# Performance work log

Measured on AMD Instinct MI355X. Metric: run time of the kernel, lower is better.

## Reference

```python
import jax, jax.numpy as jnp
import numpy as np

B, T, I, H, O = 4096, 512, 1, 64, 1


def setup_inputs() -> dict:
    key = jax.random.key(0)
    ks = jax.random.split(key, 7)
    s = 1.0 / np.sqrt(H)  # PyTorch default init scale
    return {
        "x": jax.random.normal(ks[0], (B, T, I), dtype=jnp.float32),
        "w_ih": jax.random.uniform(ks[1], (4 * H, I), jnp.float32, -s, s),
        "w_hh": jax.random.uniform(ks[2], (4 * H, H), jnp.float32, -s, s),
        "b_ih": jax.random.uniform(ks[3], (4 * H,), jnp.float32, -s, s),
        "b_hh": jax.random.uniform(ks[4], (4 * H,), jnp.float32, -s, s),
        "w_out": jax.random.uniform(ks[5], (O, H), jnp.float32, -s, s),
        "b_out": jax.random.uniform(ks[6], (O,), jnp.float32, -s, s),
    }


def reference(x, w_ih, w_hh, b_ih, b_hh, w_out, b_out):
    # x: [B, T, I]; PyTorch gate order in 4H dim is (i, f, g, o)
    b = b_ih + b_hh  # [4H]
    # precompute input projections for all timesteps: [T, B, 4H]
    xg = jnp.einsum("bti,gi->tbg", x, w_ih) + b

    def step(carry, xg_t):
        h, c = carry  # [B, H] each
        gates = xg_t + h @ w_hh.T  # [B, 4H]
        i, f, g, o = jnp.split(gates, 4, axis=-1)
        i = jax.nn.sigmoid(i)
        f = jax.nn.sigmoid(f)
        g = jnp.tanh(g)
        o = jax.nn.sigmoid(o)
        c = f * c + i * g
        h = o * jnp.tanh(c)
        return (h, c), None

    nb = x.shape[0]
    h0 = jnp.zeros((nb, w_hh.shape[1]), x.dtype)
    (h_T, _), _ = jax.lax.scan(step, (h0, h0), xg)
    # linear on last hidden state only (lstm_out[:, -1, :])
    return h_T @ w_out.T + b_out
```

## Files before the change

kernel.cpp:

```cpp
#include <hip/hip_runtime.h>


#define TT   512
#define MB   8
#define HP   72
#define BUFE (16 * HP)
#define SXP  10

#define L2E  1.4426950408889634f
#define L2E2 2.8853900817779268f

typedef _Float16 f16x8 __attribute__((ext_vector_type(8)));
typedef float    f32x4 __attribute__((ext_vector_type(4)));
typedef float    f32x2 __attribute__((ext_vector_type(2)));

#define MFMA16(a, b, c) __builtin_amdgcn_mfma_f32_16x16x32_f16((a), (b), (c), 0, 0, 0)

__device__ __forceinline__ float rcp_(float x)  { return __builtin_amdgcn_rcpf(x); }
__device__ __forceinline__ float exp2_(float x) { return __builtin_amdgcn_exp2f(x); }

__device__ __forceinline__ f16x8 cvt8s(const float4& u0, const float4& u1, float s) {
    f16x8 r;
    r[0] = (_Float16)(u0.x * s); r[1] = (_Float16)(u0.y * s);
    r[2] = (_Float16)(u0.z * s); r[3] = (_Float16)(u0.w * s);
    r[4] = (_Float16)(u1.x * s); r[5] = (_Float16)(u1.y * s);
    r[6] = (_Float16)(u1.z * s); r[7] = (_Float16)(u1.w * s);
    return r;
}

__global__ __launch_bounds__(256, 2) void lstm_mfma(
    const float* __restrict__ x,
    const float* __restrict__ w_ih,
    const float* __restrict__ w_hh,
    const float* __restrict__ b_ih,
    const float* __restrict__ b_hh,
    const float* __restrict__ w_out,
    const float* __restrict__ b_out,
    float* __restrict__ out)
{
    __shared__ __align__(16) float    sh_x[TT * SXP];
    __shared__ __align__(16) _Float16 hbuf[2 * BUFE];

    const int tid = threadIdx.x;
    const int w   = tid >> 6;
    const int L   = tid & 63;
    const int l16 = L & 15;
    const int h0  = L >> 4;
    const int b0  = blockIdx.x * MB;
    const int j   = 16 * w + l16;

    {
        const int q = tid >> 5;
        const int l = tid & 31;
        const float* xr = x + (size_t)(b0 + q) * TT;
        #pragma unroll
        for (int i = 0; i < TT / 32; ++i)
            sh_x[(l + 32 * i) * SXP + q] = xr[l + 32 * i];
    }
    for (int i = tid; i < 2 * BUFE; i += 256) hbuf[i] = (_Float16)0.0f;

    const float sc[4] = {-L2E, -L2E, L2E2, -L2E};
    f16x8 Bf[4][2];
    float wihv[4], biasv[4];
    #pragma unroll
    for (int s = 0; s < 4; ++s) {
        const int n = 64 * s + j;
        #pragma unroll
        for (int kt = 0; kt < 2; ++kt) {
            const float* p = w_hh + n * 64 + kt * 32 + h0 * 8;
            float4 u0 = *(const float4*)p;
            float4 u1 = *(const float4*)(p + 4);
            Bf[s][kt] = cvt8s(u0, u1, sc[s]);
        }
        wihv[s]  = w_ih[n] * sc[s];
        biasv[s] = (b_ih[n] + b_hh[n]) * sc[s];
    }

    const int aoff = l16 * HP + h0 * 8;
    const int xoff = 2 * h0;
    const int wr   = 4 * h0 * HP + j;

    f32x2 ccv = {0.0f, 0.0f};

    f32x4 ci[4];
    {
        const float2 x0 = *(const float2*)(sh_x + xoff);
        #pragma unroll
        for (int s = 0; s < 4; ++s) {
            ci[s][0] = fmaf(x0.x, wihv[s], biasv[s]);
            ci[s][1] = 0.0f;
            ci[s][2] = fmaf(x0.y, wihv[s], biasv[s]);
            ci[s][3] = 0.0f;
        }
    }

    __syncthreads();

    if (((blockIdx.x >> 8) ^ blockIdx.x) & 1) {
        __builtin_amdgcn_s_sleep(10);
    }

    auto step = [&](const _Float16* rb, _Float16* wb, int t) {
        f16x8 a0 = *(const f16x8*)(rb + aoff);
        f16x8 a1 = *(const f16x8*)(rb + aoff + 32);

        f32x4 acc[4];
        #pragma unroll
        for (int s = 0; s < 4; ++s)
            acc[s] = MFMA16(a1, Bf[s][1], MFMA16(a0, Bf[s][0], ci[s]));

        if (t + 1 < TT) {
            const float2 xn = *(const float2*)(sh_x + (t + 1) * SXP + xoff);
            const f32x2 xnv = {xn.x, xn.y};
            #pragma unroll
            for (int s = 0; s < 4; ++s) {
                f32x2 c2 = xnv * wihv[s] + biasv[s];
                ci[s][0] = c2[0];
                ci[s][2] = c2[1];
            }
        }

        __builtin_amdgcn_s_setprio(1);

        f32x2 Ei = {exp2_(acc[0][0]), exp2_(acc[0][2])};
        f32x2 Ef = {exp2_(acc[1][0]), exp2_(acc[1][2])};
        f32x2 Eg = {exp2_(acc[2][0]), exp2_(acc[2][2])};
        f32x2 Eo = {exp2_(acc[3][0]), exp2_(acc[3][2])};
        f32x2 Di = Ei + 1.0f, Df = Ef + 1.0f, Dg = Eg + 1.0f, Do = Eo + 1.0f;

        f32x2 FG = Df * Dg, IG = Di * Dg, IF = Di * Df;
        f32x2 P  = Di * FG;
        float u  = rcp_(P[0] * P[1]);
        f32x2 inv = {u * P[1], u * P[0]};

        f32x2 si = FG * inv, sf = IG * inv;
        f32x2 tg = 1.0f - 2.0f * (IF * inv);
        ccv = sf * ccv + si * tg;

        f32x2 ca = ccv * L2E2;
        f32x2 Ec = {exp2_(fminf(ca[0], 30.0f)), exp2_(fminf(ca[1], 30.0f))};
        f32x2 Dc = Ec + 1.0f;
        f32x2 Q  = Do * Dc;
        float v  = rcp_(Q[0] * Q[1]);
        f32x2 iq = {v * Q[1], v * Q[0]};
        f32x2 hv = (iq * Dc) * (1.0f - 2.0f * (iq * Do));

        wb[wr]          = (_Float16)hv[0];
        wb[wr + 2 * HP] = (_Float16)hv[1];

        __builtin_amdgcn_s_setprio(0);
        __syncthreads();
    };

    for (int t = 0; t < TT; t += 2) {
        step(hbuf,        hbuf + BUFE, t);
        step(hbuf + BUFE, hbuf,        t + 1);
    }

    const float wo = w_out[L];
    #pragma unroll
    for (int p = 0; p < 2; ++p) {
        const int q = 2 * w + p;
        float v = (float)hbuf[(2 * q) * HP + L] * wo;
        #pragma unroll
        for (int off = 32; off; off >>= 1) v += __shfl_down(v, off);
        if (L == 0) out[b0 + q] = v + b_out[0];
    }
}

extern "C" void kernel_launch(void* const* d_in, const int* in_sizes, int n_in,
                              void* d_out, int out_size, void* d_ws, size_t ws_size,
                              hipStream_t stream) {
    const float* x     = (const float*)d_in[0];
    const float* w_ih  = (const float*)d_in[1];
    const float* w_hh  = (const float*)d_in[2];
    const float* b_ih  = (const float*)d_in[3];
    const float* b_hh  = (const float*)d_in[4];
    const float* w_out = (const float*)d_in[5];
    const float* b_out = (const float*)d_in[6];
    float* out = (float*)d_out;

    lstm_mfma<<<4096 / MB, 256, 0, stream>>>(x, w_ih, w_hh, b_ih, b_hh,
                                             w_out, b_out, out);
}
```

Baseline: 265.9 us.

## Fill all 16 MFMA rows with batch elements, halving block count

```diff
diff --git a/kernel.cpp b/kernel.cpp
--- a/kernel.cpp
+++ b/kernel.cpp
@@ -2,10 +2,10 @@
 
 
 #define TT   512
-#define MB   8
+#define MB   16
 #define HP   72
 #define BUFE (16 * HP)
-#define SXP  10
+#define SXP  20
 
 #define L2E  1.4426950408889634f
 #define L2E2 2.8853900817779268f
@@ -28,7 +28,7 @@
     return r;
 }
 
-__global__ __launch_bounds__(256, 2) void lstm_mfma(
+__global__ __launch_bounds__(256, 1) void lstm_mfma(
     const float* __restrict__ x,
     const float* __restrict__ w_ih,
     const float* __restrict__ w_hh,
@@ -49,8 +49,9 @@
     const int b0  = blockIdx.x * MB;
     const int j   = 16 * w + l16;
 
-    {
-        const int q = tid >> 5;
+    #pragma unroll
+    for (int rep = 0; rep < 2; ++rep) {
+        const int q = (tid >> 5) + 8 * rep;
         const int l = tid & 31;
         const float* xr = x + (size_t)(b0 + q) * TT;
         #pragma unroll
@@ -77,28 +78,25 @@
     }
 
     const int aoff = l16 * HP + h0 * 8;
-    const int xoff = 2 * h0;
+    const int xb   = 4 * h0;
     const int wr   = 4 * h0 * HP + j;
 
-    f32x2 ccv = {0.0f, 0.0f};
+    f32x2 cc0 = {0.0f, 0.0f};
+    f32x2 cc1 = {0.0f, 0.0f};
 
     f32x4 ci[4];
     {
-        const float2 x0 = *(const float2*)(sh_x + xoff);
+        const float4 x0 = *(const float4*)(sh_x + xb);
         #pragma unroll
         for (int s = 0; s < 4; ++s) {
             ci[s][0] = fmaf(x0.x, wihv[s], biasv[s]);
-            ci[s][1] = 0.0f;
-            ci[s][2] = fmaf(x0.y, wihv[s], biasv[s]);
-            ci[s][3] = 0.0f;
+            ci[s][1] = fmaf(x0.y, wihv[s], biasv[s]);
+            ci[s][2] = fmaf(x0.z, wihv[s], biasv[s]);
+            ci[s][3] = fmaf(x0.w, wihv[s], biasv[s]);
         }
     }
 
     __syncthreads();
-
-    if (((blockIdx.x >> 8) ^ blockIdx.x) & 1) {
-        __builtin_amdgcn_s_sleep(10);
-    }
 
     auto step = [&](const _Float16* rb, _Float16* wb, int t) {
         f16x8 a0 = *(const f16x8*)(rb + aoff);
@@ -110,43 +108,49 @@
             acc[s] = MFMA16(a1, Bf[s][1], MFMA16(a0, Bf[s][0], ci[s]));
 
         if (t + 1 < TT) {
-            const float2 xn = *(const float2*)(sh_x + (t + 1) * SXP + xoff);
-            const f32x2 xnv = {xn.x, xn.y};
+            const float4 xn = *(const float4*)(sh_x + (t + 1) * SXP + xb);
+            const f32x2 xa = {xn.x, xn.y}, xbv = {xn.z, xn.w};
             #pragma unroll
             for (int s = 0; s < 4; ++s) {
-                f32x2 c2 = xnv * wihv[s] + biasv[s];
-                ci[s][0] = c2[0];
-                ci[s][2] = c2[1];
+                f32x2 ca2 = xa  * wihv[s] + biasv[s];
+                f32x2 cb2 = xbv * wihv[s] + biasv[s];
+                ci[s][0] = ca2[0]; ci[s][1] = ca2[1];
+                ci[s][2] = cb2[0]; ci[s][3] = cb2[1];
             }
         }
 
         __builtin_amdgcn_s_setprio(1);
 
-        f32x2 Ei = {exp2_(acc[0][0]), exp2_(acc[0][2])};
-        f32x2 Ef = {exp2_(acc[1][0]), exp2_(acc[1][2])};
-        f32x2 Eg = {exp2_(acc[2][0]), exp2_(acc[2][2])};
-        f32x2 Eo = {exp2_(acc[3][0]), exp2_(acc[3][2])};
-        f32x2 Di = Ei + 1.0f, Df = Ef + 1.0f, Dg = Eg + 1.0f, Do = Eo + 1.0f;
+        #pragma unroll
+        for (int p = 0; p < 2; ++p) {
+            f32x2& cc = p ? cc1 : cc0;
+            const int r0 = 2 * p;
+            f32x2 Ei = {exp2_(acc[0][r0]), exp2_(acc[0][r0 + 1])};
+            f32x2 Ef = {exp2_(acc[1][r0]), exp2_(acc[1][r0 + 1])};
+            f32x2 Eg = {exp2_(acc[2][r0]), exp2_(acc[2][r0 + 1])};
+            f32x2 Eo = {exp2_(acc[3][r0]), exp2_(acc[3][r0 + 1])};
+            f32x2 Di = Ei + 1.0f, Df = Ef + 1.0f, Dg = Eg + 1.0f, Do = Eo + 1.0f;
 
-        f32x2 FG = Df * Dg, IG = Di * Dg, IF = Di * Df;
-        f32x2 P  = Di * FG;
-        float u  = rcp_(P[0] * P[1]);
-        f32x2 inv = {u * P[1], u * P[0]};
+            f32x2 FG = Df * Dg, IG = Di * Dg, IF = Di * Df;
+            f32x2 P  = Di * FG;
+            float u  = rcp_(P[0] * P[1]);
+            f32x2 inv = {u * P[1], u * P[0]};
 
-        f32x2 si = FG * inv, sf = IG * inv;
-        f32x2 tg = 1.0f - 2.0f * (IF * inv);
-        ccv = sf * ccv + si * tg;
+            f32x2 si = FG * inv, sf = IG * inv;
+            f32x2 tg = 1.0f - 2.0f * (IF * inv);
+            cc = sf * cc + si * tg;
 
-        f32x2 ca = ccv * L2E2;
-        f32x2 Ec = {exp2_(fminf(ca[0], 30.0f)), exp2_(fminf(ca[1], 30.0f))};
-        f32x2 Dc = Ec + 1.0f;
-        f32x2 Q  = Do * Dc;
-        float v  = rcp_(Q[0] * Q[1]);
-        f32x2 iq = {v * Q[1], v * Q[0]};
-        f32x2 hv = (iq * Dc) * (1.0f - 2.0f * (iq * Do));
+            f32x2 ca = cc * L2E2;
+            f32x2 Ec = {exp2_(fminf(ca[0], 30.0f)), exp2_(fminf(ca[1], 30.0f))};
+            f32x2 Dc = Ec + 1.0f;
+            f32x2 Q  = Do * Dc;
+            float v  = rcp_(Q[0] * Q[1]);
+            f32x2 iq = {v * Q[1], v * Q[0]};
+            f32x2 hv = (iq * Dc) * (1.0f - 2.0f * (iq * Do));
 
-        wb[wr]          = (_Float16)hv[0];
-        wb[wr + 2 * HP] = (_Float16)hv[1];
+            wb[wr + (r0)     * HP] = (_Float16)hv[0];
+            wb[wr + (r0 + 1) * HP] = (_Float16)hv[1];
+        }
 
         __builtin_amdgcn_s_setprio(0);
         __syncthreads();
@@ -159,9 +163,9 @@
 
     const float wo = w_out[L];
     #pragma unroll
-    for (int p = 0; p < 2; ++p) {
-        const int q = 2 * w + p;
-        float v = (float)hbuf[(2 * q) * HP + L] * wo;
+    for (int p = 0; p < 4; ++p) {
+        const int q = 4 * w + p;
+        float v = (float)hbuf[q * HP + L] * wo;
         #pragma unroll
         for (int off = 32; off; off >>= 1) v += __shfl_down(v, off);
         if (L == 0) out[b0 + q] = v + b_out[0];
```

Result: slower. 325.3 us (+22.3%).
